# Performance work log

Measured on AMD Instinct MI355X. Metric: run time of the kernel, lower is better.

The kernel has to match this reference:

```python
import jax, jax.numpy as jnp
import numpy as np

VOCAB = 32000


def setup_inputs() -> dict:
    key = jax.random.key(0)
    ks = jax.random.split(key, 8)
    B, T, S, H = 8, 256, 400, 512
    return {
        "s_output": jax.random.normal(ks[0], (B, T, H), jnp.float32),
        "state_input": jax.random.normal(ks[1], (B, T, 2 * H), jnp.float32),
        "attn_scores": jax.random.uniform(ks[2], (B, T, S), jnp.float32),
        "enc_batch_extend_vocab": jax.random.randint(ks[3], (B, S), 0, VOCAB),
        "w_pgen": jax.random.normal(ks[4], (2 * H, 1), jnp.float32) * 0.02,
        "b_pgen": jnp.zeros((1,), jnp.float32),
        "w1": jax.random.normal(ks[5], (H, H), jnp.float32) * 0.02,
        "b1": jnp.zeros((H,), jnp.float32),
        "w2": jax.random.normal(ks[6], (H, VOCAB), jnp.float32) * 0.02,
        "b2": jnp.zeros((VOCAB,), jnp.float32),
    }


def reference(s_output, state_input, attn_scores, enc_batch_extend_vocab,
              w_pgen, b_pgen, w1, b1, w2, b2):
    B, T, S = attn_scores.shape
    # generation gate: sigmoid(Linear(state_input))  -> [B, T, 1]
    p_gen = jax.nn.sigmoid(state_input @ w_pgen + b_pgen)
    # vocab distribution: softmax(Linear(Linear(s_output)))  -> [B, T, V]
    logits = (s_output @ w1 + b1) @ w2 + b2
    vocab_dist = jax.nn.softmax(logits, axis=-1)
    vocab_dist_ = p_gen * vocab_dist              # [B, T, V]
    attn_dist_ = (1.0 - p_gen) * attn_scores      # [B, T, S]
    # scatter_add attention mass into vocab positions (collisions accumulate)
    bi = jnp.arange(B)[:, None, None]
    ti = jnp.arange(T)[None, :, None]
    si = enc_batch_extend_vocab[:, None, :]       # [B, 1, S] broadcasts to [B, T, S]
    final_dist = vocab_dist_.at[bi, ti, si].add(attn_dist_) + 1e-12
    return jnp.log(final_dist).reshape(-1, final_dist.shape[-1])
```

## Files before the change

kernel.cpp:

```cpp
#include <hip/hip_runtime.h>
#include <hip/hip_bf16.h>
#include <stdint.h>

#define BB 8
#define TT 256
#define SS 400
#define HH 512
#define VV 32000
#define MM (BB*TT)
#define KK 512
#define NBLK (VV/128)
#define MBLK (MM/128)
#define G2BLOCKS (NBLK*MBLK)

typedef __bf16 bf16x8 __attribute__((ext_vector_type(8)));
typedef float  f32x4  __attribute__((ext_vector_type(4)));
typedef unsigned short ushort8 __attribute__((ext_vector_type(8)));

__device__ __forceinline__ unsigned short f2bf(float x) {
    union { float f; unsigned u; } v; v.f = x;
    unsigned r = v.u + 0x7fffu + ((v.u >> 16) & 1u);
    return (unsigned short)(r >> 16);
}
__device__ __forceinline__ float bf2f(unsigned short u) {
    union { unsigned u; float f; } v; v.u = ((unsigned)u) << 16; return v.f;
}

__device__ __forceinline__ void async_ld16(const void* g, void* lds) {
    __builtin_amdgcn_global_load_lds(
        (const __attribute__((address_space(1))) unsigned int*)g,
        (__attribute__((address_space(3))) unsigned int*)lds,
        16, 0, 0);
}

__global__ __launch_bounds__(256) void f32_to_bf16_kernel(const float* __restrict__ x,
                                                          unsigned short* __restrict__ y, int n4) {
    int i = blockIdx.x * blockDim.x + threadIdx.x;
    if (i < n4) {
        float4 v = ((const float4*)x)[i];
        ushort4 o;
        o.x = f2bf(v.x); o.y = f2bf(v.y); o.z = f2bf(v.z); o.w = f2bf(v.w);
        ((ushort4*)y)[i] = o;
    }
}

__global__ __launch_bounds__(256) void transpose_bf16_kernel(const float* __restrict__ W,
                                                             unsigned short* __restrict__ Wt,
                                                             int K, int N) {
    __shared__ float tile[32][33];
    int n0 = blockIdx.x * 32, k0 = blockIdx.y * 32;
    int t = threadIdx.x;
    int r  = t >> 3;
    int c4 = (t & 7) * 4;
    float4 v = *(const float4*)(W + (size_t)(k0 + r) * N + n0 + c4);
    tile[r][c4 + 0] = v.x; tile[r][c4 + 1] = v.y;
    tile[r][c4 + 2] = v.z; tile[r][c4 + 3] = v.w;
    __syncthreads();
    ushort4 o;
    o.x = f2bf(tile[c4 + 0][r]);
    o.y = f2bf(tile[c4 + 1][r]);
    o.z = f2bf(tile[c4 + 2][r]);
    o.w = f2bf(tile[c4 + 3][r]);
    *(ushort4*)(Wt + (size_t)(n0 + r) * K + k0 + c4) = o;
}

__global__ __launch_bounds__(256) void pgen_kernel(const float* __restrict__ state,
                                                   const float* __restrict__ wp,
                                                   const float* __restrict__ bp,
                                                   float* __restrict__ pg) {
    int row  = blockIdx.x * 4 + (threadIdx.x >> 6);
    int lane = threadIdx.x & 63;
    const float* s = state + (size_t)row * (2 * HH);
    float acc = 0.f;
    for (int j = lane; j < 2 * HH; j += 64) acc += s[j] * wp[j];
    for (int off = 32; off; off >>= 1) acc += __shfl_xor(acc, off, 64);
    if (lane == 0) pg[row] = 1.f / (1.f + __expf(-(acc + bp[0])));
}

__global__ __launch_bounds__(256) void gemm1_kernel(const unsigned short* __restrict__ A,
                                                    const unsigned short* __restrict__ Bt,
                                                    const float* __restrict__ bias,
                                                    unsigned short* __restrict__ out, int N) {
    __shared__ __align__(16) unsigned short As[128 * 32];
    __shared__ __align__(16) unsigned short Bs[128 * 32];
    const int tid = threadIdx.x, wave = tid >> 6, lane = tid & 63;
    const int m0 = blockIdx.y * 128, n0 = blockIdx.x * 128;
    const int q = lane >> 4, r_ = lane & 15;
    const int wm = (wave >> 1) * 64, wn = (wave & 1) * 64;
    f32x4 acc[4][4] = {};
    for (int k0 = 0; k0 < KK; k0 += 32) {
        #pragma unroll
        for (int rr = 0; rr < 2; ++rr) {
            int cc = tid + rr * 256, row = cc >> 2, col = (cc & 3) * 8;
            async_ld16(A  + (size_t)(m0 + row) * KK + k0 + col, (char*)As + (size_t)cc * 16);
            async_ld16(Bt + (size_t)(n0 + row) * KK + k0 + col, (char*)Bs + (size_t)cc * 16);
        }
        __syncthreads();
        bf16x8 a[4], b[4];
        #pragma unroll
        for (int i = 0; i < 4; ++i) {
            a[i] = *(const bf16x8*)(As + (wm + i * 16 + r_) * 32 + q * 8);
            b[i] = *(const bf16x8*)(Bs + (wn + i * 16 + r_) * 32 + q * 8);
        }
        #pragma unroll
        for (int mi = 0; mi < 4; ++mi)
            #pragma unroll
            for (int ni = 0; ni < 4; ++ni)
                acc[mi][ni] = __builtin_amdgcn_mfma_f32_16x16x32_bf16(a[mi], b[ni], acc[mi][ni], 0, 0, 0);
        __syncthreads();
    }
    #pragma unroll
    for (int mi = 0; mi < 4; ++mi)
        #pragma unroll
        for (int ni = 0; ni < 4; ++ni) {
            int n = n0 + wn + ni * 16 + r_;
            float bv = bias[n];
            #pragma unroll
            for (int rg = 0; rg < 4; ++rg) {
                int m = m0 + wm + mi * 16 + q * 4 + rg;
                out[(size_t)m * N + n] = f2bf(acc[mi][ni][rg] + bv);
            }
        }
}

template <bool E_BF16>
__global__ __launch_bounds__(256) void gemm2_exp_kernel(const unsigned short* __restrict__ A,
                                                        const unsigned short* __restrict__ Bt,
                                                        const float* __restrict__ bias,
                                                        void* __restrict__ E,
                                                        float* __restrict__ Zpart) {
    __shared__ __align__(16) unsigned short As[128 * 32];
    __shared__ __align__(16) unsigned short Bs[128 * 32];
    __shared__ float rowsum[128];
    const int tid = threadIdx.x, wave = tid >> 6, lane = tid & 63;

    const int bid = blockIdx.x;
    const int xcd = bid & 7;
    const int sub = bid >> 3;
    const int lin = xcd * (G2BLOCKS / 8) + sub;
    const int nb  = lin >> 4;
    const int mb  = lin & 15;
    const int m0 = mb * 128, n0 = nb * 128;

    const int q = lane >> 4, r_ = lane & 15;
    const int wm = (wave >> 1) * 64, wn = (wave & 1) * 64;
    f32x4 acc[4][4] = {};
    for (int k0 = 0; k0 < KK; k0 += 32) {
        #pragma unroll
        for (int rr = 0; rr < 2; ++rr) {
            int cc = tid + rr * 256, row = cc >> 2, col = (cc & 3) * 8;
            async_ld16(A  + (size_t)(m0 + row) * KK + k0 + col, (char*)As + (size_t)cc * 16);
            async_ld16(Bt + (size_t)(n0 + row) * KK + k0 + col, (char*)Bs + (size_t)cc * 16);
        }
        __syncthreads();
        bf16x8 a[4], b[4];
        #pragma unroll
        for (int i = 0; i < 4; ++i) {
            a[i] = *(const bf16x8*)(As + (wm + i * 16 + r_) * 32 + q * 8);
            b[i] = *(const bf16x8*)(Bs + (wn + i * 16 + r_) * 32 + q * 8);
        }
        #pragma unroll
        for (int mi = 0; mi < 4; ++mi)
            #pragma unroll
            for (int ni = 0; ni < 4; ++ni)
                acc[mi][ni] = __builtin_amdgcn_mfma_f32_16x16x32_bf16(a[mi], b[ni], acc[mi][ni], 0, 0, 0);
        __syncthreads();
    }

    if (tid < 128) rowsum[tid] = 0.f;
    __syncthreads();

    float rowpart[16];
    #pragma unroll
    for (int i = 0; i < 16; ++i) rowpart[i] = 0.f;

    #pragma unroll
    for (int mi = 0; mi < 4; ++mi)
        #pragma unroll
        for (int ni = 0; ni < 4; ++ni) {
            int n = n0 + wn + ni * 16 + r_;
            float bv = bias[n];
            #pragma unroll
            for (int rg = 0; rg < 4; ++rg) {
                int m = m0 + wm + mi * 16 + q * 4 + rg;
                float e = __expf(acc[mi][ni][rg] + bv);
                if (E_BF16)
                    ((unsigned short*)E)[(size_t)m * VV + n] = f2bf(e);
                else
                    ((float*)E)[(size_t)m * VV + n] = e;
                rowpart[mi * 4 + rg] += e;
            }
        }
    #pragma unroll
    for (int i = 0; i < 16; ++i) {
        float v = rowpart[i];
        v += __shfl_xor(v, 1, 64);
        v += __shfl_xor(v, 2, 64);
        v += __shfl_xor(v, 4, 64);
        v += __shfl_xor(v, 8, 64);
        rowpart[i] = v;
    }
    if (r_ == 0) {
        #pragma unroll
        for (int mi = 0; mi < 4; ++mi)
            #pragma unroll
            for (int rg = 0; rg < 4; ++rg)
                atomicAdd(&rowsum[wm + mi * 16 + q * 4 + rg], rowpart[mi * 4 + rg]);
    }
    __syncthreads();
    if (tid < 128) Zpart[(size_t)nb * MM + m0 + tid] = rowsum[tid];
}

__global__ __launch_bounds__(256) void zfinal_kernel(const float* __restrict__ Zpart,
                                                     float* __restrict__ Z) {
    int row = blockIdx.x * 256 + threadIdx.x;
    float s = 0.f;
    for (int nb = 0; nb < NBLK; ++nb) s += Zpart[(size_t)nb * MM + row];
    Z[row] = s;
}

template <bool E_BF16>
__global__ __launch_bounds__(256) void finalize_kernel(const void* __restrict__ E,
                                                       float* __restrict__ out,
                                                       const float* __restrict__ pg_arr,
                                                       const float* __restrict__ Z,
                                                       const float* __restrict__ attn,
                                                       const int* __restrict__ enc) {
    constexpr int CH = VV / 8;
    __shared__ float acc[CH];
    int bid = blockIdx.x;
    int row = bid >> 3;
    int part = bid & 7;
    int nbase = part * CH;
    f32x4* acc4 = (f32x4*)acc;
    for (int j = threadIdx.x; j < CH / 4; j += 256) acc4[j] = (f32x4){0.f, 0.f, 0.f, 0.f};
    float pg = pg_arr[row];
    float scale = pg / Z[row];
    float om = 1.f - pg;
    int batch = row / TT;
    __syncthreads();
    for (int s = threadIdx.x; s < SS; s += 256) {
        int idx = enc[batch * SS + s];
        if (idx >= nbase && idx < nbase + CH)
            atomicAdd(&acc[idx - nbase], om * attn[(size_t)row * SS + s]);
    }
    __syncthreads();
    size_t base = (size_t)row * VV + nbase;
    for (int j = threadIdx.x * 8; j < CH; j += 2048) {
        float e[8];
        if (E_BF16) {
            ushort8 u = *(const ushort8*)((const unsigned short*)E + base + j);
            #pragma unroll
            for (int i = 0; i < 8; ++i) e[i] = bf2f(u[i]);
        } else {
            f32x4 u0 = *(const f32x4*)((const float*)E + base + j);
            f32x4 u1 = *(const f32x4*)((const float*)E + base + j + 4);
            e[0]=u0[0]; e[1]=u0[1]; e[2]=u0[2]; e[3]=u0[3];
            e[4]=u1[0]; e[5]=u1[1]; e[6]=u1[2]; e[7]=u1[3];
        }
        f32x4 a0 = acc4[(j >> 2) + 0];
        f32x4 a1 = acc4[(j >> 2) + 1];
        f32x4 o0, o1;
        #pragma unroll
        for (int i = 0; i < 4; ++i) o0[i] = __logf(scale * e[i]     + a0[i] + 1e-12f);
        #pragma unroll
        for (int i = 0; i < 4; ++i) o1[i] = __logf(scale * e[4 + i] + a1[i] + 1e-12f);
        *(f32x4*)(out + base + j)     = o0;
        *(f32x4*)(out + base + j + 4) = o1;
    }
}

extern "C" void kernel_launch(void* const* d_in, const int* in_sizes, int n_in,
                              void* d_out, int out_size, void* d_ws, size_t ws_size,
                              hipStream_t stream) {
    const float* s_output = (const float*)d_in[0];
    const float* state_in = (const float*)d_in[1];
    const float* attn     = (const float*)d_in[2];
    const int*   enc      = (const int*)  d_in[3];
    const float* w_pgen   = (const float*)d_in[4];
    const float* b_pgen   = (const float*)d_in[5];
    const float* w1       = (const float*)d_in[6];
    const float* b1       = (const float*)d_in[7];
    const float* w2       = (const float*)d_in[8];
    const float* b2       = (const float*)d_in[9];

    char* ws = (char*)d_ws;
    float*          pg     = (float*)(ws + 0);
    float*          Z      = (float*)(ws + 8192);
    unsigned short* hidden = (unsigned short*)(ws + 16384);
    unsigned short* sA     = (unsigned short*)(ws + 2113536);
    float*          Zpart  = (float*)(ws + 2113536);
    unsigned short* w1t    = (unsigned short*)(ws + 4210688);
    unsigned short* w2t    = (unsigned short*)(ws + 4734976);
    unsigned short* Ebf    = (unsigned short*)(ws + 37502976);

    const size_t NEED_BIG = 37502976ull + 2ull * MM * VV;
    const bool big = (ws_size >= NEED_BIG);

    f32_to_bf16_kernel<<<(MM * HH / 4 + 255) / 256, 256, 0, stream>>>(s_output, sA, MM * HH / 4);
    transpose_bf16_kernel<<<dim3(HH / 32, KK / 32), 256, 0, stream>>>(w1, w1t, KK, HH);
    transpose_bf16_kernel<<<dim3(VV / 32, KK / 32), 256, 0, stream>>>(w2, w2t, KK, VV);
    pgen_kernel<<<MM / 4, 256, 0, stream>>>(state_in, w_pgen, b_pgen, pg);
    gemm1_kernel<<<dim3(HH / 128, MM / 128), 256, 0, stream>>>(sA, w1t, b1, hidden, HH);

    if (big) {
        gemm2_exp_kernel<true><<<G2BLOCKS, 256, 0, stream>>>(hidden, w2t, b2, Ebf, Zpart);
        zfinal_kernel<<<MM / 256, 256, 0, stream>>>(Zpart, Z);
        finalize_kernel<true><<<MM * 8, 256, 0, stream>>>(Ebf, (float*)d_out, pg, Z, attn, enc);
    } else {
        gemm2_exp_kernel<false><<<G2BLOCKS, 256, 0, stream>>>(hidden, w2t, b2, d_out, Zpart);
        zfinal_kernel<<<MM / 256, 256, 0, stream>>>(Zpart, Z);
        finalize_kernel<false><<<MM * 8, 256, 0, stream>>>(d_out, (float*)d_out, pg, Z, attn, enc);
    }
}
```

Before: 523.2 us.

## Enlarge vocab GEMM tiles to 256x256x64 with swizzled double-buffered LDS pipeline

Rewrites the second GEMM-plus-exp kernel to use 256x256 output tiles with a K-step of 64 and 512 threads per block. A/B tiles are loaded asynchronously into two XOR-swizzled LDS buffers so the next K-slice streams in while the current one feeds MFMA, with wave priority raised around the MFMA bursts. The aim is more operand reuse per byte loaded, fewer LDS bank conflicts and fewer bank-stalled barriers. The cost is about 128KB of LDS per block, which limits occupancy to one block per CU, plus heavier register pressure from the 8x4 accumulators. The row-sum reduction and partial-Z count are adjusted to the new tile shape.

Result: faster. 511.5 us (-2.2%).

```diff
diff --git a/kernel.cpp b/kernel.cpp
--- a/kernel.cpp
+++ b/kernel.cpp
@@ -9,9 +9,13 @@
 #define VV 32000
 #define MM (BB*TT)
 #define KK 512
-#define NBLK (VV/128)
-#define MBLK (MM/128)
-#define G2BLOCKS (NBLK*MBLK)
+
+#define BM2 256
+#define BN2 256
+#define BK2 64
+#define NBLK2 (VV/BN2)
+#define MBLK2 (MM/BM2)
+#define G2B (NBLK2*MBLK2)
 
 typedef __bf16 bf16x8 __attribute__((ext_vector_type(8)));
 typedef float  f32x4  __attribute__((ext_vector_type(4)));
@@ -124,98 +128,133 @@
 }
 
 template <bool E_BF16>
-__global__ __launch_bounds__(256) void gemm2_exp_kernel(const unsigned short* __restrict__ A,
-                                                        const unsigned short* __restrict__ Bt,
-                                                        const float* __restrict__ bias,
-                                                        void* __restrict__ E,
-                                                        float* __restrict__ Zpart) {
-    __shared__ __align__(16) unsigned short As[128 * 32];
-    __shared__ __align__(16) unsigned short Bs[128 * 32];
-    __shared__ float rowsum[128];
+__global__ __launch_bounds__(512, 2) void gemm2_exp_kernel(const unsigned short* __restrict__ A,
+                                                           const unsigned short* __restrict__ Bt,
+                                                           const float* __restrict__ bias,
+                                                           void* __restrict__ E,
+                                                           float* __restrict__ Zpart) {
+    __shared__ __align__(16) char lds[2][65536];
     const int tid = threadIdx.x, wave = tid >> 6, lane = tid & 63;
+    const int q = lane >> 4, r_ = lane & 15;
+    const int wm = wave >> 2;
+    const int wn = wave & 3;
 
     const int bid = blockIdx.x;
     const int xcd = bid & 7;
     const int sub = bid >> 3;
-    const int lin = xcd * (G2BLOCKS / 8) + sub;
-    const int nb  = lin >> 4;
-    const int mb  = lin & 15;
-    const int m0 = mb * 128, n0 = nb * 128;
-
-    const int q = lane >> 4, r_ = lane & 15;
-    const int wm = (wave >> 1) * 64, wn = (wave & 1) * 64;
-    f32x4 acc[4][4] = {};
-    for (int k0 = 0; k0 < KK; k0 += 32) {
-        #pragma unroll
-        for (int rr = 0; rr < 2; ++rr) {
-            int cc = tid + rr * 256, row = cc >> 2, col = (cc & 3) * 8;
-            async_ld16(A  + (size_t)(m0 + row) * KK + k0 + col, (char*)As + (size_t)cc * 16);
-            async_ld16(Bt + (size_t)(n0 + row) * KK + k0 + col, (char*)Bs + (size_t)cc * 16);
-        }
-        __syncthreads();
-        bf16x8 a[4], b[4];
-        #pragma unroll
-        for (int i = 0; i < 4; ++i) {
-            a[i] = *(const bf16x8*)(As + (wm + i * 16 + r_) * 32 + q * 8);
-            b[i] = *(const bf16x8*)(Bs + (wn + i * 16 + r_) * 32 + q * 8);
-        }
-        #pragma unroll
-        for (int mi = 0; mi < 4; ++mi)
-            #pragma unroll
-            for (int ni = 0; ni < 4; ++ni)
-                acc[mi][ni] = __builtin_amdgcn_mfma_f32_16x16x32_bf16(a[mi], b[ni], acc[mi][ni], 0, 0, 0);
-        __syncthreads();
-    }
-
-    if (tid < 128) rowsum[tid] = 0.f;
-    __syncthreads();
-
-    float rowpart[16];
+    const int lin = xcd * (G2B / 8) + sub;
+    const int nb  = lin >> 3;
+    const int mb  = lin & 7;
+    const int m0 = mb * BM2, n0 = nb * BN2;
+
+    f32x4 acc[8][4] = {};
+
+    auto stage = [&](int t, int j) {
+        int c   = tid + j * 512;
+        int row = c >> 3;
+        int colb = (c & 7) * 16;
+        int src  = colb ^ ((row & 7) << 4);
+        char* base = lds[t & 1];
+        async_ld16((const char*)A  + ((size_t)(m0 + row) * KK + t * BK2) * 2 + src,
+                   base + c * 16);
+        async_ld16((const char*)Bt + ((size_t)(n0 + row) * KK + t * BK2) * 2 + src,
+                   base + 32768 + c * 16);
+    };
+
     #pragma unroll
-    for (int i = 0; i < 16; ++i) rowpart[i] = 0.f;
-
+    for (int j = 0; j < 4; ++j) stage(0, j);
+    asm volatile("s_waitcnt vmcnt(0)" ::: "memory");
+    __builtin_amdgcn_s_barrier();
+    __builtin_amdgcn_sched_barrier(0);
+
+    for (int t = 0; t < KK / BK2; ++t) {
+        char* buf = lds[t & 1];
+        #pragma unroll
+        for (int p = 0; p < 4; ++p) {
+            if (t < KK / BK2 - 1) stage(t + 1, p);
+            const int mib = (p >> 1) * 4;
+            const int nib = (p & 1) * 2;
+            bf16x8 af[4][2], bg[2][2];
+            #pragma unroll
+            for (int mi = 0; mi < 4; ++mi)
+                #pragma unroll
+                for (int ks = 0; ks < 2; ++ks) {
+                    int row = wm * 128 + (mib + mi) * 16 + r_;
+                    int cb  = (ks * 64 + q * 16) ^ ((row & 7) << 4);
+                    af[mi][ks] = *(const bf16x8*)(buf + row * 128 + cb);
+                }
+            #pragma unroll
+            for (int ni = 0; ni < 2; ++ni)
+                #pragma unroll
+                for (int ks = 0; ks < 2; ++ks) {
+                    int row = wn * 64 + (nib + ni) * 16 + r_;
+                    int cb  = (ks * 64 + q * 16) ^ ((row & 7) << 4);
+                    bg[ni][ks] = *(const bf16x8*)(buf + 32768 + row * 128 + cb);
+                }
+            __builtin_amdgcn_s_setprio(1);
+            #pragma unroll
+            for (int mi = 0; mi < 4; ++mi)
+                #pragma unroll
+                for (int ni = 0; ni < 2; ++ni)
+                    #pragma unroll
+                    for (int ks = 0; ks < 2; ++ks)
+                        acc[mib + mi][nib + ni] = __builtin_amdgcn_mfma_f32_16x16x32_bf16(
+                            af[mi][ks], bg[ni][ks], acc[mib + mi][nib + ni], 0, 0, 0);
+            __builtin_amdgcn_s_setprio(0);
+            __builtin_amdgcn_sched_barrier(0);
+            __builtin_amdgcn_s_barrier();
+            __builtin_amdgcn_sched_barrier(0);
+        }
+        asm volatile("s_waitcnt vmcnt(0)" ::: "memory");
+        __builtin_amdgcn_sched_barrier(0);
+        __builtin_amdgcn_s_barrier();
+        __builtin_amdgcn_sched_barrier(0);
+    }
+
+    float* rowsum = (float*)&lds[0][0];
+    if (tid < BM2) rowsum[tid] = 0.f;
+    __syncthreads();
+
+    float bv[4];
     #pragma unroll
-    for (int mi = 0; mi < 4; ++mi)
+    for (int ni = 0; ni < 4; ++ni) bv[ni] = bias[n0 + wn * 64 + ni * 16 + r_];
+
+    #pragma unroll
+    for (int mi = 0; mi < 8; ++mi) {
+        float rp[4] = {0.f, 0.f, 0.f, 0.f};
         #pragma unroll
         for (int ni = 0; ni < 4; ++ni) {
-            int n = n0 + wn + ni * 16 + r_;
-            float bv = bias[n];
+            int n = n0 + wn * 64 + ni * 16 + r_;
             #pragma unroll
             for (int rg = 0; rg < 4; ++rg) {
-                int m = m0 + wm + mi * 16 + q * 4 + rg;
-                float e = __expf(acc[mi][ni][rg] + bv);
+                int m = m0 + wm * 128 + mi * 16 + q * 4 + rg;
+                float e = __expf(acc[mi][ni][rg] + bv[ni]);
                 if (E_BF16)
                     ((unsigned short*)E)[(size_t)m * VV + n] = f2bf(e);
                 else
                     ((float*)E)[(size_t)m * VV + n] = e;
-                rowpart[mi * 4 + rg] += e;
+                rp[rg] += e;
             }
         }
-    #pragma unroll
-    for (int i = 0; i < 16; ++i) {
-        float v = rowpart[i];
-        v += __shfl_xor(v, 1, 64);
-        v += __shfl_xor(v, 2, 64);
-        v += __shfl_xor(v, 4, 64);
-        v += __shfl_xor(v, 8, 64);
-        rowpart[i] = v;
-    }
-    if (r_ == 0) {
-        #pragma unroll
-        for (int mi = 0; mi < 4; ++mi)
-            #pragma unroll
-            for (int rg = 0; rg < 4; ++rg)
-                atomicAdd(&rowsum[wm + mi * 16 + q * 4 + rg], rowpart[mi * 4 + rg]);
-    }
-    __syncthreads();
-    if (tid < 128) Zpart[(size_t)nb * MM + m0 + tid] = rowsum[tid];
+        #pragma unroll
+        for (int rg = 0; rg < 4; ++rg) {
+            float v = rp[rg];
+            v += __shfl_xor(v, 1, 64);
+            v += __shfl_xor(v, 2, 64);
+            v += __shfl_xor(v, 4, 64);
+            v += __shfl_xor(v, 8, 64);
+            if (r_ == 0) atomicAdd(&rowsum[wm * 128 + mi * 16 + q * 4 + rg], v);
+        }
+    }
+    __syncthreads();
+    if (tid < BM2) Zpart[(size_t)nb * MM + m0 + tid] = rowsum[tid];
 }
 
 __global__ __launch_bounds__(256) void zfinal_kernel(const float* __restrict__ Zpart,
                                                      float* __restrict__ Z) {
     int row = blockIdx.x * 256 + threadIdx.x;
     float s = 0.f;
-    for (int nb = 0; nb < NBLK; ++nb) s += Zpart[(size_t)nb * MM + row];
+    for (int nb = 0; nb < NBLK2; ++nb) s += Zpart[(size_t)nb * MM + row];
     Z[row] = s;
 }
 
@@ -304,11 +343,11 @@
     gemm1_kernel<<<dim3(HH / 128, MM / 128), 256, 0, stream>>>(sA, w1t, b1, hidden, HH);
 
     if (big) {
-        gemm2_exp_kernel<true><<<G2BLOCKS, 256, 0, stream>>>(hidden, w2t, b2, Ebf, Zpart);
+        gemm2_exp_kernel<true><<<G2B, 512, 0, stream>>>(hidden, w2t, b2, Ebf, Zpart);
         zfinal_kernel<<<MM / 256, 256, 0, stream>>>(Zpart, Z);
         finalize_kernel<true><<<MM * 8, 256, 0, stream>>>(Ebf, (float*)d_out, pg, Z, attn, enc);
     } else {
-        gemm2_exp_kernel<false><<<G2BLOCKS, 256, 0, stream>>>(hidden, w2t, b2, d_out, Zpart);
+        gemm2_exp_kernel<false><<<G2B, 512, 0, stream>>>(hidden, w2t, b2, d_out, Zpart);
         zfinal_kernel<<<MM / 256, 256, 0, stream>>>(Zpart, Z);
         finalize_kernel<false><<<MM * 8, 256, 0, stream>>>(d_out, (float*)d_out, pg, Z, attn, enc);
     }
```
